# Optimization experiments

Hardware: AMD Instinct MI355X
Metric: run time of the kernel (lower is better)

The kernel has to match this reference:

```python
import jax, jax.numpy as jnp
import numpy as np

N_NODES = 100000
N_EDGES = 1600000
D = 64


def setup_inputs() -> dict:
    key = jax.random.key(0)
    k1, k2, k3, k4 = jax.random.split(key, 4)
    x = jax.random.normal(k1, (N_NODES, D), dtype=jnp.float32)
    # glorot-uniform scale for Linear weight [out_dim, in_dim]
    stdv = np.sqrt(6.0 / (D + D)).astype(np.float32)
    W = jax.random.uniform(k2, (D, D), dtype=jnp.float32, minval=-stdv, maxval=stdv)
    bias = jnp.zeros((D,), dtype=jnp.float32)  # forward() uses a zero bias
    edge_index = jax.random.randint(k3, (2, N_EDGES), 0, N_NODES, dtype=jnp.int64)
    counts = jax.random.randint(k4, (N_NODES,), 0, 16, dtype=jnp.int64)
    out_edge_index = jnp.arange(N_EDGES, dtype=jnp.int64)
    return {"x": x, "W": W, "bias": bias, "edge_index": edge_index,
            "counts": counts, "out_edge_index": out_edge_index, "layer_i": 0}


def reference(x, W, bias, edge_index, counts, out_edge_index, layer_i):
    # GCN layer: y = x @ W^T; gather by source; scatter-sum by destination; add bias.
    # counts / out_edge_index / layer_i are layout hints for the fused CUDA kernel
    # (mygraph.gcn) and do not change the math.
    y = x @ W.T                              # [N, D_out]
    src = edge_index[0]                      # [E]
    dst = edge_index[1]                      # [E]
    msgs = y[src]                            # [E, D_out] edge gather
    out = jax.ops.segment_sum(msgs, dst, num_segments=x.shape[0])  # [N, D_out]
    return out + bias
```

## Files before the change

kernel.cpp:

```cpp
#include <hip/hip_runtime.h>


#define DIM 64
#define BN 64
#define BN_SHIFT 6
#define BN_MASK 63
#define NB_MAX 2048
#define PB 256
#define CAP 1536

__device__ __forceinline__ unsigned short f32_to_bf16_rne(float f) {
    unsigned u = __float_as_uint(f);
    unsigned r = u + 0x7FFFu + ((u >> 16) & 1u);
    return (unsigned short)(r >> 16);
}

__global__ __launch_bounds__(1024) void convert_hist_kernel(
        const float* __restrict__ x, const int* __restrict__ ei,
        ushort4* __restrict__ xb4, int* __restrict__ scanbuf,
        int E, int N, int nb, int total4) {
    __shared__ int h[NB_MAX];
    const int t = threadIdx.x;
    const int bid = blockIdx.x;

    for (int b = t; b < nb; b += 1024) h[b] = 0;
    __syncthreads();

    for (int i = bid * 1024 + t; i < total4; i += PB * 1024) {
        float4 v = ((const float4*)x)[i];
        ushort4 o;
        o.x = f32_to_bf16_rne(v.x); o.y = f32_to_bf16_rne(v.y);
        o.z = f32_to_bf16_rne(v.z); o.w = f32_to_bf16_rne(v.w);
        xb4[i] = o;
    }
    if (bid == 0 && t < 16) {
        ushort4 z; z.x = 0; z.y = 0; z.z = 0; z.w = 0;
        xb4[(size_t)N * 16 + t] = z;
    }

    for (int e = bid * 1024 + t; e < E; e += PB * 1024)
        atomicAdd(&h[ei[E + e] >> BN_SHIFT], 1);
    __syncthreads();
    for (int b = t; b < nb; b += 1024)
        scanbuf[b * PB + bid] = h[b];
}

__global__ __launch_bounds__(256) void rowscan_kernel(
        int* __restrict__ buf, int* __restrict__ rowtot, int nb) {
    const int lane = threadIdx.x & 63;
    const int row = blockIdx.x * 4 + (threadIdx.x >> 6);
    if (row >= nb) return;

    int4* r = (int4*)(buf + (size_t)row * PB);
    int4 v = r[lane];
    int s0 = v.x, s1 = s0 + v.y, s2 = s1 + v.z, s3 = s2 + v.w;
    int ls = s3;
    int incl = ls;
    #pragma unroll
    for (int d = 1; d < 64; d <<= 1) {
        int u = __shfl_up(incl, d, 64);
        if (lane >= d) incl += u;
    }
    int excl = incl - ls;
    int4 w;
    w.x = excl; w.y = excl + s0; w.z = excl + s1; w.w = excl + s2;
    r[lane] = w;
    if (lane == 63) rowtot[row] = incl;
}

__global__ __launch_bounds__(512) void basescan_kernel(
        const int* __restrict__ rowtot, int* __restrict__ gbase, int nb, int E) {
    __shared__ int tot[NB_MAX];
    __shared__ int tmp[512];
    const int t = threadIdx.x;
    for (int j = t; j < NB_MAX; j += 512) tot[j] = (j < nb) ? rowtot[j] : 0;
    __syncthreads();
    int c0 = tot[4 * t + 0], c1 = tot[4 * t + 1];
    int c2 = tot[4 * t + 2], c3 = tot[4 * t + 3];
    int s4 = c0 + c1 + c2 + c3;
    tmp[t] = s4;
    __syncthreads();
    #pragma unroll
    for (int d = 1; d < 512; d <<= 1) {
        int u = (t >= d) ? tmp[t - d] : 0;
        __syncthreads();
        tmp[t] += u;
        __syncthreads();
    }
    int excl = tmp[t] - s4;
    if (4 * t + 0 < nb) gbase[4 * t + 0] = excl;
    if (4 * t + 1 < nb) gbase[4 * t + 1] = excl + c0;
    if (4 * t + 2 < nb) gbase[4 * t + 2] = excl + c0 + c1;
    if (4 * t + 3 < nb) gbase[4 * t + 3] = excl + c0 + c1 + c2;
    if (t == 0) gbase[nb] = E;
}

__global__ __launch_bounds__(1024) void scatter_kernel(
        const int* __restrict__ ei, const int* __restrict__ scanbuf,
        const int* __restrict__ gbase, int* __restrict__ binned, int E, int nb) {
    __shared__ int curs[NB_MAX];
    const int t = threadIdx.x;
    const int bid = blockIdx.x;

    for (int b = t; b < nb; b += 1024)
        curs[b] = gbase[b] + scanbuf[b * PB + bid];
    __syncthreads();

    for (int e = bid * 1024 + t; e < E; e += PB * 1024) {
        int s = ei[e];
        int d = ei[E + e];
        int p = atomicAdd(&curs[d >> BN_SHIFT], 1);
        binned[p] = (s << BN_SHIFT) | (d & BN_MASK);
    }
}

__device__ __forceinline__ void acc8(float (&a)[8], const uint4& v) {
    a[0] += __uint_as_float(v.x << 16); a[1] += __uint_as_float(v.x & 0xFFFF0000u);
    a[2] += __uint_as_float(v.y << 16); a[3] += __uint_as_float(v.y & 0xFFFF0000u);
    a[4] += __uint_as_float(v.z << 16); a[5] += __uint_as_float(v.z & 0xFFFF0000u);
    a[6] += __uint_as_float(v.w << 16); a[7] += __uint_as_float(v.w & 0xFFFF0000u);
}

__device__ __forceinline__ float epilogue64(const float (&a)[8],
                                            const float (&wv)[DIM], float bb) {
    float r0 = bb, r1 = 0.f, r2 = 0.f, r3 = 0.f;
    #pragma unroll
    for (int k = 0; k < DIM; k += 4) {
        r0 += __int_as_float(__builtin_amdgcn_readlane(
                  __float_as_int(a[(k + 0) & 7]), (k + 0) >> 3)) * wv[k + 0];
        r1 += __int_as_float(__builtin_amdgcn_readlane(
                  __float_as_int(a[(k + 1) & 7]), (k + 1) >> 3)) * wv[k + 1];
        r2 += __int_as_float(__builtin_amdgcn_readlane(
                  __float_as_int(a[(k + 2) & 7]), (k + 2) >> 3)) * wv[k + 2];
        r3 += __int_as_float(__builtin_amdgcn_readlane(
                  __float_as_int(a[(k + 3) & 7]), (k + 3) >> 3)) * wv[k + 3];
    }
    return (r0 + r1) + (r2 + r3);
}

__global__ __launch_bounds__(256) void sort_gather_kernel(
        const unsigned short* __restrict__ xh, const int* __restrict__ binned,
        const int* __restrict__ gbase, int* __restrict__ gsrcs,
        const float* __restrict__ W, const float* __restrict__ bias,
        float* __restrict__ out, int N, int E) {
    __shared__ int cnt[BN];
    __shared__ int basel[BN + 1];
    __shared__ int tmp[BN];
    __shared__ int slds[CAP];

    const int t = threadIdx.x;
    const int g = blockIdx.x;
    const int lane = t & 63;
    const int wid = t >> 6;
    const int node0 = g << BN_SHIFT;

    float wv[DIM];
    #pragma unroll
    for (int k4 = 0; k4 < DIM / 4; ++k4) {
        float4 tw = *(const float4*)(W + (size_t)lane * DIM + k4 * 4);
        wv[k4 * 4 + 0] = tw.x; wv[k4 * 4 + 1] = tw.y;
        wv[k4 * 4 + 2] = tw.z; wv[k4 * 4 + 3] = tw.w;
    }
    const float bb = bias[lane];

    const int seg0 = gbase[g];
    const int seg1 = gbase[g + 1];
    const int total = seg1 - seg0;

    if (t < BN) cnt[t] = 0;
    __syncthreads();

    for (int i = seg0 + t; i < seg1; i += 256)
        atomicAdd(&cnt[binned[i] & BN_MASK], 1);
    __syncthreads();

    int myv = (t < BN) ? cnt[t] : 0;
    if (t < BN) tmp[t] = myv;
    __syncthreads();
    #pragma unroll
    for (int d = 1; d < BN; d <<= 1) {
        int u = (t < BN && t >= d) ? tmp[t - d] : 0;
        __syncthreads();
        if (t < BN) tmp[t] += u;
        __syncthreads();
    }
    if (t < BN) basel[t] = tmp[t] - myv;
    if (t == BN - 1) basel[BN] = tmp[t];
    if (t < BN) cnt[t] = tmp[t] - myv;
    __syncthreads();

    const bool fits = (total <= CAP);
    if (fits) {
        for (int i = seg0 + t; i < seg1; i += 256) {
            int v = binned[i];
            int p = atomicAdd(&cnt[v & BN_MASK], 1);
            slds[p] = v >> BN_SHIFT;
        }
    } else {
        for (int i = seg0 + t; i < seg1; i += 256) {
            int v = binned[i];
            int p = atomicAdd(&cnt[v & BN_MASK], 1);
            gsrcs[seg0 + p] = v >> BN_SHIFT;
        }
    }
    __syncthreads();

    const int sub8 = lane >> 3;
    const int fb   = (lane & 7) << 3;
    const int zrow = N;
    const int slast = E + 48;
    for (int q = wid; q < (BN >> 2); q += 4) {
        const int nl = q << 2;
        int b0 = basel[nl + 0], e0 = basel[nl + 1];
        int b1 = basel[nl + 1], e1 = basel[nl + 2];
        int b2 = basel[nl + 2], e2 = basel[nl + 3];
        int b3 = basel[nl + 3], e3 = basel[nl + 4];
        int c0 = (e0 - b0 + 7) >> 3, c1 = (e1 - b1 + 7) >> 3;
        int c2 = (e2 - b2 + 7) >> 3, c3 = (e3 - b3 + 7) >> 3;
        int cmax = max(max(c0, c1), max(c2, c3));
        cmax = __builtin_amdgcn_readfirstlane(cmax);

        float A0[8] = {0.f,0.f,0.f,0.f,0.f,0.f,0.f,0.f};
        float A1[8] = {0.f,0.f,0.f,0.f,0.f,0.f,0.f,0.f};
        float A2[8] = {0.f,0.f,0.f,0.f,0.f,0.f,0.f,0.f};
        float A3[8] = {0.f,0.f,0.f,0.f,0.f,0.f,0.f,0.f};

        if (fits) {
            for (int c = 0; c < cmax; ++c) {
                const int o = (c << 3) + sub8;
                int i0 = b0 + o, i1 = b1 + o, i2 = b2 + o, i3 = b3 + o;
                int s0 = slds[min(i0, CAP - 1)];
                int s1 = slds[min(i1, CAP - 1)];
                int s2 = slds[min(i2, CAP - 1)];
                int s3 = slds[min(i3, CAP - 1)];
                s0 = (i0 < e0) ? s0 : zrow;
                s1 = (i1 < e1) ? s1 : zrow;
                s2 = (i2 < e2) ? s2 : zrow;
                s3 = (i3 < e3) ? s3 : zrow;
                uint4 v0 = *(const uint4*)(xh + (size_t)s0 * DIM + fb);
                uint4 v1 = *(const uint4*)(xh + (size_t)s1 * DIM + fb);
                uint4 v2 = *(const uint4*)(xh + (size_t)s2 * DIM + fb);
                uint4 v3 = *(const uint4*)(xh + (size_t)s3 * DIM + fb);
                acc8(A0, v0); acc8(A1, v1); acc8(A2, v2); acc8(A3, v3);
            }
        } else {
            for (int c = 0; c < cmax; ++c) {
                const int o = (c << 3) + sub8;
                int i0 = b0 + o, i1 = b1 + o, i2 = b2 + o, i3 = b3 + o;
                int s0 = gsrcs[min(seg0 + i0, slast)];
                int s1 = gsrcs[min(seg0 + i1, slast)];
                int s2 = gsrcs[min(seg0 + i2, slast)];
                int s3 = gsrcs[min(seg0 + i3, slast)];
                s0 = (i0 < e0) ? s0 : zrow;
                s1 = (i1 < e1) ? s1 : zrow;
                s2 = (i2 < e2) ? s2 : zrow;
                s3 = (i3 < e3) ? s3 : zrow;
                uint4 v0 = *(const uint4*)(xh + (size_t)s0 * DIM + fb);
                uint4 v1 = *(const uint4*)(xh + (size_t)s1 * DIM + fb);
                uint4 v2 = *(const uint4*)(xh + (size_t)s2 * DIM + fb);
                uint4 v3 = *(const uint4*)(xh + (size_t)s3 * DIM + fb);
                acc8(A0, v0); acc8(A1, v1); acc8(A2, v2); acc8(A3, v3);
            }
        }

        #pragma unroll
        for (int d = 8; d <= 32; d <<= 1) {
            #pragma unroll
            for (int j = 0; j < 8; ++j) {
                A0[j] += __shfl_xor(A0[j], d, 64);
                A1[j] += __shfl_xor(A1[j], d, 64);
                A2[j] += __shfl_xor(A2[j], d, 64);
                A3[j] += __shfl_xor(A3[j], d, 64);
            }
        }

        const int n0 = node0 + nl;
        if (n0 + 0 < N) out[(size_t)(n0 + 0) * DIM + lane] = epilogue64(A0, wv, bb);
        if (n0 + 1 < N) out[(size_t)(n0 + 1) * DIM + lane] = epilogue64(A1, wv, bb);
        if (n0 + 2 < N) out[(size_t)(n0 + 2) * DIM + lane] = epilogue64(A2, wv, bb);
        if (n0 + 3 < N) out[(size_t)(n0 + 3) * DIM + lane] = epilogue64(A3, wv, bb);
    }
}

__global__ void gcn_scatter_kernel(const float* __restrict__ x,
                                   const int* __restrict__ edge_index,
                                   float* __restrict__ out, int n_edges) {
    int gid = blockIdx.x * blockDim.x + threadIdx.x;
    int e = gid >> 4;
    if (e >= n_edges) return;
    int j = (gid & 15) << 2;
    int src = edge_index[e];
    int dst = edge_index[n_edges + e];
    const float4 v = *(const float4*)(x + (size_t)src * DIM + j);
    float* o = out + (size_t)dst * DIM + j;
    atomicAdd(o + 0, v.x); atomicAdd(o + 1, v.y);
    atomicAdd(o + 2, v.z); atomicAdd(o + 3, v.w);
}

__global__ void gcn_linear_inplace_kernel(float* __restrict__ out,
                                          const float* __restrict__ W,
                                          const float* __restrict__ bias,
                                          int n_nodes) {
    __shared__ float Wt[DIM * DIM];
    __shared__ float rows[4][DIM];
    int tid = threadIdx.x;
    int col = tid & 63;
    int r = tid >> 6;
    for (int i = tid; i < DIM * DIM; i += 256) {
        int c = i >> 6, k = i & 63;
        Wt[k * DIM + c] = W[i];
    }
    int row = blockIdx.x * 4 + r;
    if (row < n_nodes) rows[r][col] = out[(size_t)row * DIM + col];
    __syncthreads();
    if (row < n_nodes) {
        float a = 0.f;
        #pragma unroll
        for (int k = 0; k < DIM; ++k) a += rows[r][k] * Wt[k * DIM + col];
        out[(size_t)row * DIM + col] = a + bias[col];
    }
}

extern "C" void kernel_launch(void* const* d_in, const int* in_sizes, int n_in,
                              void* d_out, int out_size, void* d_ws, size_t ws_size,
                              hipStream_t stream) {
    const float* x          = (const float*)d_in[0];
    const float* W          = (const float*)d_in[1];
    const float* bias       = (const float*)d_in[2];
    const int*   edge_index = (const int*)d_in[3];

    const int E = in_sizes[3] / 2;
    const int N = in_sizes[0] / DIM;
    float* out = (float*)d_out;

    const int nb = (N + BN - 1) >> BN_SHIFT;

    auto align256 = [](size_t v) { return (v + 255) & ~(size_t)255; };
    const size_t xb_b   = align256(((size_t)N + 1) * DIM * 2);
    const size_t bin_b  = align256((size_t)E * 4);
    const size_t scan_b = align256((size_t)nb * PB * 4);
    const size_t rt_b   = align256((size_t)nb * 4);
    const size_t gb_b   = align256(((size_t)nb + 1) * 4);
    const size_t srcs_b = align256(((size_t)E + 64) * 4);
    const size_t needA = xb_b + bin_b + scan_b + rt_b + gb_b + srcs_b;

    if (nb <= NB_MAX && N < (1 << 24) && ws_size >= needA) {
        char* p = (char*)d_ws;
        ushort4* xb4 = (ushort4*)p;          p += xb_b;
        int* binned  = (int*)p;              p += bin_b;
        int* scanbuf = (int*)p;              p += scan_b;
        int* rowtot  = (int*)p;              p += rt_b;
        int* gbase   = (int*)p;              p += gb_b;
        int* gsrcs   = (int*)p;

        const int total4 = N * DIM / 4;

        convert_hist_kernel<<<PB, 1024, 0, stream>>>(
            x, edge_index, xb4, scanbuf, E, N, nb, total4);
        rowscan_kernel<<<(nb + 3) / 4, 256, 0, stream>>>(scanbuf, rowtot, nb);
        basescan_kernel<<<1, 512, 0, stream>>>(rowtot, gbase, nb, E);
        scatter_kernel<<<PB, 1024, 0, stream>>>(
            edge_index, scanbuf, gbase, binned, E, nb);
        sort_gather_kernel<<<nb, 256, 0, stream>>>(
            (const unsigned short*)xb4, binned, gbase, gsrcs, W, bias, out, N, E);
    } else {
        hipMemsetAsync(d_out, 0, (size_t)out_size * sizeof(float), stream);
        long long total = (long long)E * 16;
        int grid = (int)((total + 255) / 256);
        gcn_scatter_kernel<<<grid, 256, 0, stream>>>(x, edge_index, out, E);
        int lgrid = (N + 3) / 4;
        gcn_linear_inplace_kernel<<<lgrid, 256, 0, stream>>>(out, W, bias, N);
    }
}
```

Measured before the change: 212.5 us.

## Replace global scan with fixed-capacity bins and overflow fixup path

Drops the exact two-level prefix scan (rowscan, basescan, separate scatter kernel) and gives each 64-node bin a fixed slot of CAPE entries. Slot offsets come from one global atomicAdd per bin per block, so histogram and scatter fuse into one prep kernel. Edges that overflow a bin go to a side buffer, which a new fixup kernel applies with fp32 atomics after the gather. This cuts three launches and a pass over the edge list, at the cost of a memset, a padded binned array, and an extra (usually empty) fixup launch. Bin slot order now depends on atomic timing, so fp32 sums are no longer deterministic.

```diff
diff --git a/kernel.cpp b/kernel.cpp
--- a/kernel.cpp
+++ b/kernel.cpp
@@ -7,7 +7,8 @@
 #define BN_MASK 63
 #define NB_MAX 2048
 #define PB 256
-#define CAP 1536
+#define CAPE 1536
+#define OVF_MAX 262144
 
 __device__ __forceinline__ unsigned short f32_to_bf16_rne(float f) {
     unsigned u = __float_as_uint(f);
@@ -15,10 +16,11 @@
     return (unsigned short)(r >> 16);
 }
 
-__global__ __launch_bounds__(1024) void convert_hist_kernel(
+__global__ __launch_bounds__(1024) void fused_prep_kernel(
         const float* __restrict__ x, const int* __restrict__ ei,
-        ushort4* __restrict__ xb4, int* __restrict__ scanbuf,
-        int E, int N, int nb, int total4) {
+        ushort4* __restrict__ xb4, int* __restrict__ gcnt,
+        int* __restrict__ binned, int* __restrict__ ovf,
+        int* __restrict__ ovfcnt, int E, int N, int nb, int total4) {
     __shared__ int h[NB_MAX];
     const int t = threadIdx.x;
     const int bid = blockIdx.x;
@@ -41,76 +43,26 @@
     for (int e = bid * 1024 + t; e < E; e += PB * 1024)
         atomicAdd(&h[ei[E + e] >> BN_SHIFT], 1);
     __syncthreads();
-    for (int b = t; b < nb; b += 1024)
-        scanbuf[b * PB + bid] = h[b];
-}
-
-__global__ __launch_bounds__(256) void rowscan_kernel(
-        int* __restrict__ buf, int* __restrict__ rowtot, int nb) {
-    const int lane = threadIdx.x & 63;
-    const int row = blockIdx.x * 4 + (threadIdx.x >> 6);
-    if (row >= nb) return;
-
-    int4* r = (int4*)(buf + (size_t)row * PB);
-    int4 v = r[lane];
-    int s0 = v.x, s1 = s0 + v.y, s2 = s1 + v.z, s3 = s2 + v.w;
-    int ls = s3;
-    int incl = ls;
-    #pragma unroll
-    for (int d = 1; d < 64; d <<= 1) {
-        int u = __shfl_up(incl, d, 64);
-        if (lane >= d) incl += u;
-    }
-    int excl = incl - ls;
-    int4 w;
-    w.x = excl; w.y = excl + s0; w.z = excl + s1; w.w = excl + s2;
-    r[lane] = w;
-    if (lane == 63) rowtot[row] = incl;
-}
-
-__global__ __launch_bounds__(512) void basescan_kernel(
-        const int* __restrict__ rowtot, int* __restrict__ gbase, int nb, int E) {
-    __shared__ int tot[NB_MAX];
-    __shared__ int tmp[512];
-    const int t = threadIdx.x;
-    for (int j = t; j < NB_MAX; j += 512) tot[j] = (j < nb) ? rowtot[j] : 0;
-    __syncthreads();
-    int c0 = tot[4 * t + 0], c1 = tot[4 * t + 1];
-    int c2 = tot[4 * t + 2], c3 = tot[4 * t + 3];
-    int s4 = c0 + c1 + c2 + c3;
-    tmp[t] = s4;
-    __syncthreads();
-    #pragma unroll
-    for (int d = 1; d < 512; d <<= 1) {
-        int u = (t >= d) ? tmp[t - d] : 0;
-        __syncthreads();
-        tmp[t] += u;
-        __syncthreads();
-    }
-    int excl = tmp[t] - s4;
-    if (4 * t + 0 < nb) gbase[4 * t + 0] = excl;
-    if (4 * t + 1 < nb) gbase[4 * t + 1] = excl + c0;
-    if (4 * t + 2 < nb) gbase[4 * t + 2] = excl + c0 + c1;
-    if (4 * t + 3 < nb) gbase[4 * t + 3] = excl + c0 + c1 + c2;
-    if (t == 0) gbase[nb] = E;
-}
-
-__global__ __launch_bounds__(1024) void scatter_kernel(
-        const int* __restrict__ ei, const int* __restrict__ scanbuf,
-        const int* __restrict__ gbase, int* __restrict__ binned, int E, int nb) {
-    __shared__ int curs[NB_MAX];
-    const int t = threadIdx.x;
-    const int bid = blockIdx.x;
-
-    for (int b = t; b < nb; b += 1024)
-        curs[b] = gbase[b] + scanbuf[b * PB + bid];
+
+    for (int b = t; b < nb; b += 1024) {
+        int c = h[b];
+        int base = 0;
+        if (c > 0) base = atomicAdd(&gcnt[b], c);
+        h[b] = b * CAPE + base;
+    }
     __syncthreads();
 
     for (int e = bid * 1024 + t; e < E; e += PB * 1024) {
         int s = ei[e];
         int d = ei[E + e];
-        int p = atomicAdd(&curs[d >> BN_SHIFT], 1);
-        binned[p] = (s << BN_SHIFT) | (d & BN_MASK);
+        int b = d >> BN_SHIFT;
+        int p = atomicAdd(&h[b], 1);
+        if (p < b * CAPE + CAPE) {
+            binned[p] = (s << BN_SHIFT) | (d & BN_MASK);
+        } else {
+            int q = atomicAdd(ovfcnt, 1);
+            if (q < OVF_MAX) { ovf[2 * q] = s; ovf[2 * q + 1] = d; }
+        }
     }
 }
 
@@ -140,13 +92,12 @@
 
 __global__ __launch_bounds__(256) void sort_gather_kernel(
         const unsigned short* __restrict__ xh, const int* __restrict__ binned,
-        const int* __restrict__ gbase, int* __restrict__ gsrcs,
-        const float* __restrict__ W, const float* __restrict__ bias,
-        float* __restrict__ out, int N, int E) {
+        const int* __restrict__ gcnt, const float* __restrict__ W,
+        const float* __restrict__ bias, float* __restrict__ out, int N) {
     __shared__ int cnt[BN];
     __shared__ int basel[BN + 1];
     __shared__ int tmp[BN];
-    __shared__ int slds[CAP];
+    __shared__ int slds[CAPE];
 
     const int t = threadIdx.x;
     const int g = blockIdx.x;
@@ -163,9 +114,10 @@
     }
     const float bb = bias[lane];
 
-    const int seg0 = gbase[g];
-    const int seg1 = gbase[g + 1];
-    const int total = seg1 - seg0;
+    const int seg0 = g * CAPE;
+    int len = gcnt[g];
+    if (len > CAPE) len = CAPE;
+    const int seg1 = seg0 + len;
 
     if (t < BN) cnt[t] = 0;
     __syncthreads();
@@ -189,26 +141,16 @@
     if (t < BN) cnt[t] = tmp[t] - myv;
     __syncthreads();
 
-    const bool fits = (total <= CAP);
-    if (fits) {
-        for (int i = seg0 + t; i < seg1; i += 256) {
-            int v = binned[i];
-            int p = atomicAdd(&cnt[v & BN_MASK], 1);
-            slds[p] = v >> BN_SHIFT;
-        }
-    } else {
-        for (int i = seg0 + t; i < seg1; i += 256) {
-            int v = binned[i];
-            int p = atomicAdd(&cnt[v & BN_MASK], 1);
-            gsrcs[seg0 + p] = v >> BN_SHIFT;
-        }
+    for (int i = seg0 + t; i < seg1; i += 256) {
+        int v = binned[i];
+        int p = atomicAdd(&cnt[v & BN_MASK], 1);
+        slds[p] = v >> BN_SHIFT;
     }
     __syncthreads();
 
     const int sub8 = lane >> 3;
     const int fb   = (lane & 7) << 3;
     const int zrow = N;
-    const int slast = E + 48;
     for (int q = wid; q < (BN >> 2); q += 4) {
         const int nl = q << 2;
         int b0 = basel[nl + 0], e0 = basel[nl + 1];
@@ -225,42 +167,22 @@
         float A2[8] = {0.f,0.f,0.f,0.f,0.f,0.f,0.f,0.f};
         float A3[8] = {0.f,0.f,0.f,0.f,0.f,0.f,0.f,0.f};
 
-        if (fits) {
-            for (int c = 0; c < cmax; ++c) {
-                const int o = (c << 3) + sub8;
-                int i0 = b0 + o, i1 = b1 + o, i2 = b2 + o, i3 = b3 + o;
-                int s0 = slds[min(i0, CAP - 1)];
-                int s1 = slds[min(i1, CAP - 1)];
-                int s2 = slds[min(i2, CAP - 1)];
-                int s3 = slds[min(i3, CAP - 1)];
-                s0 = (i0 < e0) ? s0 : zrow;
-                s1 = (i1 < e1) ? s1 : zrow;
-                s2 = (i2 < e2) ? s2 : zrow;
-                s3 = (i3 < e3) ? s3 : zrow;
-                uint4 v0 = *(const uint4*)(xh + (size_t)s0 * DIM + fb);
-                uint4 v1 = *(const uint4*)(xh + (size_t)s1 * DIM + fb);
-                uint4 v2 = *(const uint4*)(xh + (size_t)s2 * DIM + fb);
-                uint4 v3 = *(const uint4*)(xh + (size_t)s3 * DIM + fb);
-                acc8(A0, v0); acc8(A1, v1); acc8(A2, v2); acc8(A3, v3);
-            }
-        } else {
-            for (int c = 0; c < cmax; ++c) {
-                const int o = (c << 3) + sub8;
-                int i0 = b0 + o, i1 = b1 + o, i2 = b2 + o, i3 = b3 + o;
-                int s0 = gsrcs[min(seg0 + i0, slast)];
-                int s1 = gsrcs[min(seg0 + i1, slast)];
-                int s2 = gsrcs[min(seg0 + i2, slast)];
-                int s3 = gsrcs[min(seg0 + i3, slast)];
-                s0 = (i0 < e0) ? s0 : zrow;
-                s1 = (i1 < e1) ? s1 : zrow;
-                s2 = (i2 < e2) ? s2 : zrow;
-                s3 = (i3 < e3) ? s3 : zrow;
-                uint4 v0 = *(const uint4*)(xh + (size_t)s0 * DIM + fb);
-                uint4 v1 = *(const uint4*)(xh + (size_t)s1 * DIM + fb);
-                uint4 v2 = *(const uint4*)(xh + (size_t)s2 * DIM + fb);
-                uint4 v3 = *(const uint4*)(xh + (size_t)s3 * DIM + fb);
-                acc8(A0, v0); acc8(A1, v1); acc8(A2, v2); acc8(A3, v3);
-            }
+        for (int c = 0; c < cmax; ++c) {
+            const int o = (c << 3) + sub8;
+            int i0 = b0 + o, i1 = b1 + o, i2 = b2 + o, i3 = b3 + o;
+            int s0 = slds[min(i0, CAPE - 1)];
+            int s1 = slds[min(i1, CAPE - 1)];
+            int s2 = slds[min(i2, CAPE - 1)];
+            int s3 = slds[min(i3, CAPE - 1)];
+            s0 = (i0 < e0) ? s0 : zrow;
+            s1 = (i1 < e1) ? s1 : zrow;
+            s2 = (i2 < e2) ? s2 : zrow;
+            s3 = (i3 < e3) ? s3 : zrow;
+            uint4 v0 = *(const uint4*)(xh + (size_t)s0 * DIM + fb);
+            uint4 v1 = *(const uint4*)(xh + (size_t)s1 * DIM + fb);
+            uint4 v2 = *(const uint4*)(xh + (size_t)s2 * DIM + fb);
+            uint4 v3 = *(const uint4*)(xh + (size_t)s3 * DIM + fb);
+            acc8(A0, v0); acc8(A1, v1); acc8(A2, v2); acc8(A3, v3);
         }
 
         #pragma unroll
@@ -279,6 +201,40 @@
         if (n0 + 1 < N) out[(size_t)(n0 + 1) * DIM + lane] = epilogue64(A1, wv, bb);
         if (n0 + 2 < N) out[(size_t)(n0 + 2) * DIM + lane] = epilogue64(A2, wv, bb);
         if (n0 + 3 < N) out[(size_t)(n0 + 3) * DIM + lane] = epilogue64(A3, wv, bb);
+    }
+}
+
+__global__ __launch_bounds__(256) void fixup_kernel(
+        const float* __restrict__ x, const int* __restrict__ ovf,
+        const int* __restrict__ ovfcnt, const float* __restrict__ W,
+        float* __restrict__ out) {
+    int cnt = *ovfcnt;
+    if (cnt > OVF_MAX) cnt = OVF_MAX;
+    if (cnt == 0) return;
+    const int lane = threadIdx.x & 63;
+    const int gwave = (blockIdx.x * blockDim.x + threadIdx.x) >> 6;
+    const int total_waves = (gridDim.x * blockDim.x) >> 6;
+
+    float wv[DIM];
+    #pragma unroll
+    for (int k4 = 0; k4 < DIM / 4; ++k4) {
+        float4 tw = *(const float4*)(W + (size_t)lane * DIM + k4 * 4);
+        wv[k4 * 4 + 0] = tw.x; wv[k4 * 4 + 1] = tw.y;
+        wv[k4 * 4 + 2] = tw.z; wv[k4 * 4 + 3] = tw.w;
+    }
+    for (int i = gwave; i < cnt; i += total_waves) {
+        int s = ovf[2 * i];
+        int d = ovf[2 * i + 1];
+        float v = x[(size_t)s * DIM + lane];
+        float r0 = 0.f, r1 = 0.f, r2 = 0.f, r3 = 0.f;
+        #pragma unroll
+        for (int k = 0; k < DIM; k += 4) {
+            r0 += __int_as_float(__builtin_amdgcn_readlane(__float_as_int(v), k + 0)) * wv[k + 0];
+            r1 += __int_as_float(__builtin_amdgcn_readlane(__float_as_int(v), k + 1)) * wv[k + 1];
+            r2 += __int_as_float(__builtin_amdgcn_readlane(__float_as_int(v), k + 2)) * wv[k + 2];
+            r3 += __int_as_float(__builtin_amdgcn_readlane(__float_as_int(v), k + 3)) * wv[k + 3];
+        }
+        atomicAdd(&out[(size_t)d * DIM + lane], (r0 + r1) + (r2 + r3));
     }
 }
 
@@ -337,32 +293,27 @@
 
     auto align256 = [](size_t v) { return (v + 255) & ~(size_t)255; };
     const size_t xb_b   = align256(((size_t)N + 1) * DIM * 2);
-    const size_t bin_b  = align256((size_t)E * 4);
-    const size_t scan_b = align256((size_t)nb * PB * 4);
-    const size_t rt_b   = align256((size_t)nb * 4);
-    const size_t gb_b   = align256(((size_t)nb + 1) * 4);
-    const size_t srcs_b = align256(((size_t)E + 64) * 4);
-    const size_t needA = xb_b + bin_b + scan_b + rt_b + gb_b + srcs_b;
+    const size_t bin_b  = align256((size_t)nb * CAPE * 4);
+    const size_t cnt_b  = align256(((size_t)nb + 64) * 4);
+    const size_t ovf_b  = align256((size_t)OVF_MAX * 2 * 4);
+    const size_t needA = xb_b + bin_b + cnt_b + ovf_b;
 
     if (nb <= NB_MAX && N < (1 << 24) && ws_size >= needA) {
         char* p = (char*)d_ws;
         ushort4* xb4 = (ushort4*)p;          p += xb_b;
         int* binned  = (int*)p;              p += bin_b;
-        int* scanbuf = (int*)p;              p += scan_b;
-        int* rowtot  = (int*)p;              p += rt_b;
-        int* gbase   = (int*)p;              p += gb_b;
-        int* gsrcs   = (int*)p;
+        int* gcnt    = (int*)p;              p += cnt_b;
+        int* ovf     = (int*)p;
+        int* ovfcnt  = gcnt + nb;
 
         const int total4 = N * DIM / 4;
 
-        convert_hist_kernel<<<PB, 1024, 0, stream>>>(
-            x, edge_index, xb4, scanbuf, E, N, nb, total4);
-        rowscan_kernel<<<(nb + 3) / 4, 256, 0, stream>>>(scanbuf, rowtot, nb);
-        basescan_kernel<<<1, 512, 0, stream>>>(rowtot, gbase, nb, E);
-        scatter_kernel<<<PB, 1024, 0, stream>>>(
-            edge_index, scanbuf, gbase, binned, E, nb);
+        hipMemsetAsync(gcnt, 0, cnt_b, stream);
+        fused_prep_kernel<<<PB, 1024, 0, stream>>>(
+            x, edge_index, xb4, gcnt, binned, ovf, ovfcnt, E, N, nb, total4);
         sort_gather_kernel<<<nb, 256, 0, stream>>>(
-            (const unsigned short*)xb4, binned, gbase, gsrcs, W, bias, out, N, E);
+            (const unsigned short*)xb4, binned, gcnt, W, bias, out, N);
+        fixup_kernel<<<64, 256, 0, stream>>>(x, ovf, ovfcnt, W, out);
     } else {
         hipMemsetAsync(d_out, 0, (size_t)out_size * sizeof(float), stream);
         long long total = (long long)E * 16;
```

New measurement: 199.7 us. 1.06x faster.
